# Performance work log

Hardware: AMD Instinct MI355X
Metric: run time of the kernel (lower is better)

## Reference

```python
import jax, jax.numpy as jnp
import numpy as np

DEMO_T = 4
N_HEADS = 4
N_LAYERS = 2
EPS = 1e-5
IN_DIM = 512
FF_DIM = 128
TEMP = float(np.sqrt(IN_DIM))  # temperature=None -> sqrt(in_dim)


def setup_inputs() -> dict:
    key = jax.random.key(0)
    ks = jax.random.split(key, 12)
    B, d, T, H, W = 8, IN_DIM, 36, 7, 12
    s_in = 1.0 / np.sqrt(d)
    s_ff = 1.0 / np.sqrt(FF_DIM)
    f32 = jnp.float32
    return {
        "inputs": jax.random.normal(ks[0], (B, d, T, H, W), f32),
        "demo_wq": jax.random.normal(ks[1], (N_LAYERS, FF_DIM, d), f32) * s_in,
        "demo_wk": jax.random.normal(ks[2], (N_LAYERS, FF_DIM, d), f32) * s_in,
        "demo_wv": jax.random.normal(ks[3], (N_LAYERS, FF_DIM, d), f32) * s_in,
        "demo_wo": jax.random.normal(ks[4], (N_LAYERS, d, FF_DIM), f32) * s_ff,
        "obs_wq": jax.random.normal(ks[5], (N_LAYERS, FF_DIM, d), f32) * s_in,
        "obs_wk": jax.random.normal(ks[6], (N_LAYERS, FF_DIM, d), f32) * s_in,
        "obs_wv": jax.random.normal(ks[7], (N_LAYERS, FF_DIM, d), f32) * s_in,
        "obs_wo": jax.random.normal(ks[8], (N_LAYERS, d, FF_DIM), f32) * s_ff,
        "bn_gamma": jnp.ones((N_LAYERS, d), f32),
        "bn_beta": jnp.zeros((N_LAYERS, d), f32),
    }


def _conv1x1(w, x):
    # 1x1x1 Conv3d, bias=False == per-voxel channel mixing
    return jnp.einsum('od,bdthw->bothw', w, x)


def _forward(inputs, demo_wq, demo_wk, demo_wv, demo_wo,
             obs_wq, obs_wk, obs_wv, obs_wo, bn_gamma, bn_beta):
    B, d, T, H, W = inputs.shape
    HW = H * W
    obs_T = T - DEMO_T
    neg_inf = jnp.asarray(-jnp.inf, inputs.dtype)
    # causal log-mask over demo tokens, block-expanded to spatial positions
    tril = jnp.tril(jnp.ones((DEMO_T, DEMO_T), inputs.dtype))
    mask = jnp.repeat(jnp.repeat(tril, HW, axis=0), HW, axis=1)  # (dTHW, dTHW)
    log_mask = jnp.where(mask > 0, jnp.asarray(0.0, inputs.dtype), neg_inf)

    x = inputs
    for i in range(N_LAYERS):
        demo_in = x[:, :, :DEMO_T]   # [B,d,dT,H,W]
        obs_in = x[:, :, DEMO_T:]    # [B,d,oT,H,W]

        # --- demo self-attention (causal) ---
        def demo_heads(w):
            y = _conv1x1(w, demo_in)                      # [B,ff,dT,H,W]
            return y.reshape(B, N_HEADS, -1, DEMO_T * HW)  # [B,n,ch,dTHW]
        dq, dk, dv = demo_heads(demo_wq[i]), demo_heads(demo_wk[i]), demo_heads(demo_wv[i])
        dkq = jnp.einsum('bnci,bncj->bnij', dk, dq) / TEMP + log_mask
        dattn = jax.nn.softmax(dkq, axis=-1)               # softmax over j (as in source)
        dv_att = jnp.einsum('bncj,bnij->bnci', dv, dattn)  # attended demo values
        # NOTE: the source computes demo_out via demo_Outs + relu-skip but never
        # uses it downstream (dead code); only dv_att/dk feed the obs fusion.

        # --- obs attention, fused with demo keys/attended-values ---
        def obs_heads(w):
            y = _conv1x1(w, obs_in)                        # [B,ff,oT,H,W]
            y = y.reshape(B, N_HEADS, -1, obs_T, HW)
            return jnp.transpose(y, (0, 3, 1, 2, 4))       # [B,oT,n,ch,HW]
        oq, ok, ov = obs_heads(obs_wq[i]), obs_heads(obs_wk[i]), obs_heads(obs_wv[i])
        rep_k = jnp.broadcast_to(dk[:, None], (B, obs_T) + dk.shape[1:])
        rep_v = jnp.broadcast_to(dv_att[:, None], (B, obs_T) + dv_att.shape[1:])
        cat_k = jnp.concatenate([rep_k, ok], axis=-1)      # [B,oT,n,ch,(1+dT)HW]
        cat_v = jnp.concatenate([rep_v, ov], axis=-1)
        okq = jnp.einsum('btnci,btncj->btnij', cat_k, oq) / TEMP  # i=cat len, j=HW
        oattn = jax.nn.softmax(okq, axis=-1)               # softmax over j (source: dim=4)
        ov_att = jnp.einsum('btncj,btnji->btnci', cat_v, oattn)  # [B,oT,n,ch,HW]
        obs_out = _conv1x1(obs_wo[i],
                           jnp.transpose(ov_att, (0, 2, 3, 1, 4)).reshape(B, -1, obs_T, H, W))
        # skip (out_dim == in_dim), dropout=0 -> identity
        obs_res = obs_in + jax.nn.relu(obs_out)

        # shared BatchNorm3d (training-mode batch stats) over concatenated streams
        x = jnp.concatenate([demo_in, obs_res], axis=2)
        mean = x.mean(axis=(0, 2, 3, 4)).reshape(1, -1, 1, 1, 1)
        var = x.var(axis=(0, 2, 3, 4)).reshape(1, -1, 1, 1, 1)
        g = bn_gamma[i].reshape(1, -1, 1, 1, 1)
        b = bn_beta[i].reshape(1, -1, 1, 1, 1)
        x = g * (x - mean) * jax.lax.rsqrt(var + EPS) + b
    return x  # == out_dict['last']


def reference(inputs, demo_wq, demo_wk, demo_wv, demo_wo,
              obs_wq, obs_wk, obs_wv, obs_wo, bn_gamma, bn_beta):
    return _forward(inputs, demo_wq, demo_wk, demo_wv, demo_wo,
                    obs_wq, obs_wk, obs_wv, obs_wo, bn_gamma, bn_beta)
```

## Files before the change

kernel.cpp:

```cpp
#include <hip/hip_runtime.h>

#define B_N 8
#define D_N 512
#define T_N 36
#define HW_N 84
#define THW_N 3024
#define DT_N 4
#define OT_N 32
#define NH_N 4
#define FF_N 128
#define CH_N 32
#define DI_N 336
#define OI_N 2688
#define CAT_N 420
#define INV_TEMP 0.04419417382415922f
#define BN_EPS 1e-5f
#define INV_CNT (1.0f / 24192.0f)

#define SW_DWQ 0
#define SW_DWK 131072
#define SW_DWV 262144
#define SW_OWQ 393216
#define SW_OWK 524288
#define SW_OWV 655360
#define SW_OWO 786432
#define S_DQ   917504
#define S_DK   1261568
#define S_DV   1605632
#define S_DVA  1949696
#define S_OQ   2293760
#define S_OK   5046272
#define S_OV   7798784
#define S_OVA  10551296
#define S_XBF  13303808

typedef short bf16x8 __attribute__((ext_vector_type(8)));
typedef float f32x4 __attribute__((ext_vector_type(4)));
typedef unsigned int u32;

#define GLD16(SRC, DST) __builtin_amdgcn_global_load_lds( \
    (const __attribute__((address_space(1))) u32*)(SRC), \
    (__attribute__((address_space(3))) u32*)(DST), 16, 0, 0)

__device__ __forceinline__ short f2bf(float f) {
    unsigned u = __float_as_uint(f);
    u += 0x7fffu + ((u >> 16) & 1u);
    return (short)(u >> 16);
}
__device__ __forceinline__ float bf2f(short s) {
    return __uint_as_float(((unsigned)(unsigned short)s) << 16);
}

__global__ __launch_bounds__(256) void cvt_w_kernel(
    const float* __restrict__ s0, const float* __restrict__ s1,
    const float* __restrict__ s2, const float* __restrict__ s3,
    const float* __restrict__ s4, const float* __restrict__ s5,
    const float* __restrict__ s6, short* __restrict__ dst,
    float* __restrict__ stats)
{
    const int bid = blockIdx.x;
    if (bid == 0) {
        #pragma unroll
        for (int k = 0; k < 8; ++k) stats[threadIdx.x * 8 + k] = 0.f;
    }
    const int a = bid >> 6, blk = bid & 63;
    const float* src;
    switch (a) {
        case 0: src = s0; break; case 1: src = s1; break;
        case 2: src = s2; break; case 3: src = s3; break;
        case 4: src = s4; break; case 5: src = s5; break;
        default: src = s6;
    }
    const int idx = (blk * 256 + (int)threadIdx.x) * 8;
    float4 f0 = *reinterpret_cast<const float4*>(src + idx);
    float4 f1 = *reinterpret_cast<const float4*>(src + idx + 4);
    bf16x8 pk;
    pk[0] = f2bf(f0.x); pk[1] = f2bf(f0.y); pk[2] = f2bf(f0.z); pk[3] = f2bf(f0.w);
    pk[4] = f2bf(f1.x); pk[5] = f2bf(f1.y); pk[6] = f2bf(f1.z); pk[7] = f2bf(f1.w);
    size_t dstoff;
    if (a < 6) {
        const int layer = idx >> 16;
        const int w = idx & 65535;
        const int mg = w >> 9;
        const int k  = w & 511;
        const int p  = k >> 6;
        const int kc = (k >> 3) & 7;
        const int mh = mg >> 6;
        const int m  = mg & 63;
        dstoff = (size_t)layer * 65536 +
                 (size_t)(((p * 2 + mh) * 8 + kc) * 64 + m) * 8;
    } else {
        dstoff = idx;
    }
    *reinterpret_cast<bf16x8*>(dst + (size_t)a * 131072 + dstoff) = pk;
}

__global__ __launch_bounds__(256) void xin_kernel(
    const float* __restrict__ in_f, short* __restrict__ xbf,
    float* __restrict__ stats0)
{
    __shared__ short tile[48][65];
    __shared__ float red_s[16][64];
    __shared__ float red_q[16][64];

    const int bid = blockIdx.x;
    const int b = bid / 504, rem = bid % 504, tt = rem >> 3, cblk = rem & 7;
    const int t0 = tt * 48, c0 = cblk * 64;
    const int tid = threadIdx.x;
    const bool is_demo = (tt < 7);

    #pragma unroll
    for (int l0 = 0; l0 < 768; l0 += 256) {
        int l = l0 + tid;
        int cc = l / 12, tg = l % 12;
        size_t addr = ((size_t)b * D_N + c0 + cc) * THW_N + t0 + tg * 4;
        float4 v = *reinterpret_cast<const float4*>(in_f + addr);
        tile[tg * 4 + 0][cc] = f2bf(v.x);
        tile[tg * 4 + 1][cc] = f2bf(v.y);
        tile[tg * 4 + 2][cc] = f2bf(v.z);
        tile[tg * 4 + 3][cc] = f2bf(v.w);
    }
    __syncthreads();
    float psum[4] = {}, psq[4] = {};
    const int cg = tid & 15;
    #pragma unroll
    for (int l0 = 0; l0 < 768; l0 += 256) {
        int l = l0 + tid;
        int tk = l >> 4;
        short4 s4;
        s4.x = tile[tk][cg * 4 + 0];
        s4.y = tile[tk][cg * 4 + 1];
        s4.z = tile[tk][cg * 4 + 2];
        s4.w = tile[tk][cg * 4 + 3];
        *reinterpret_cast<short4*>(
            xbf + ((size_t)b * THW_N + t0 + tk) * 512 + c0 + cg * 4) = s4;
        if (is_demo) {
            float v0 = bf2f(s4.x), v1 = bf2f(s4.y), v2 = bf2f(s4.z), v3 = bf2f(s4.w);
            psum[0] += v0; psum[1] += v1; psum[2] += v2; psum[3] += v3;
            psq[0] += v0 * v0; psq[1] += v1 * v1; psq[2] += v2 * v2; psq[3] += v3 * v3;
        }
    }
    if (!is_demo) return;
    __syncthreads();
    #pragma unroll
    for (int j = 0; j < 4; ++j) {
        red_s[tid >> 4][cg * 4 + j] = psum[j];
        red_q[tid >> 4][cg * 4 + j] = psq[j];
    }
    __syncthreads();
    if (tid < 64) {
        float s = 0.f, q = 0.f;
        #pragma unroll
        for (int r = 0; r < 16; ++r) { s += red_s[r][tid]; q += red_q[r][tid]; }
        atomicAdd(&stats0[c0 + tid], s);
        atomicAdd(&stats0[512 + c0 + tid], q);
    }
}

__global__ __launch_bounds__(256) void proj_mfma_kernel(
    const short* __restrict__ xbf, short* __restrict__ ws, int layer)
{
    __shared__ short As[3][4096];
    __shared__ short Bs[3072];

    const int tid = threadIdx.x;
    const int lane = tid & 63, wv = tid >> 6;
    const int l15 = lane & 15, q = lane >> 4;

    const int bid = blockIdx.x;
    const int mh = bid & 1;
    const int rem = bid >> 1;
    const int b = rem / 63, ct = rem - b * 63;
    const bool is_demo = (ct < 7);
    const int woff = layer * 65536;
    const short* W0 = ws + (is_demo ? SW_DWQ : SW_OWQ) + woff;
    const short* W1 = ws + (is_demo ? SW_DWK : SW_OWK) + woff;
    const short* W2 = ws + (is_demo ? SW_DWV : SW_OWV) + woff;
    const int Ltok = is_demo ? DI_N : OI_N;
    const int colL = is_demo ? ct * 48 : (ct - 7) * 48;
    short* Yq = ws + (is_demo ? S_DQ : S_OQ);
    short* Yk = ws + (is_demo ? S_DK : S_OK);
    short* Yv = ws + (is_demo ? S_DV : S_OV);
    const short* Xb = xbf + ((size_t)b * THW_N + (is_demo ? 0 : DI_N) + colL) * 512;

    const short* rp[3];
    rp[0] = W0 + (size_t)mh * 4096 + lane * 8;
    rp[1] = W1 + (size_t)mh * 4096 + lane * 8;
    rp[2] = W2 + (size_t)mh * 4096 + lane * 8;
    const short* bp[2];
    #pragma unroll
    for (int h = 0; h < 2; ++h) {
        int c = h * 192 + wv * 64 + lane;
        bp[h] = Xb + (size_t)(c % 48) * 512 + (c / 48) * 8;
    }

    f32x4 acc[3][3] = {};

    for (int k0 = 0; k0 < D_N; k0 += 64) {
        const size_t poff = (size_t)(k0 >> 6) * 8192;
        __syncthreads();
        #pragma unroll
        for (int h = 0; h < 2; ++h) {
            #pragma unroll
            for (int wt = 0; wt < 3; ++wt)
                GLD16(rp[wt] + poff + (h * 256 + wv * 64) * 8,
                      &As[wt][(h * 256 + wv * 64) * 8]);
        }
        if (wv < 3) {
            GLD16(bp[0] + k0, &Bs[(wv * 64) * 8]);
            GLD16(bp[1] + k0, &Bs[(192 + wv * 64) * 8]);
        }
        __syncthreads();

        #pragma unroll
        for (int kk = 0; kk < 2; ++kk) {
            const int kc = kk * 4 + q;
            bf16x8 bfr[3];
            #pragma unroll
            for (int nt = 0; nt < 3; ++nt)
                bfr[nt] = *reinterpret_cast<const bf16x8*>(
                    &Bs[(kc * 48 + nt * 16 + l15) * 8]);
            #pragma unroll
            for (int wt = 0; wt < 3; ++wt) {
                bf16x8 afr = *reinterpret_cast<const bf16x8*>(
                    &As[wt][(kc * 64 + wv * 16 + l15) * 8]);
                #pragma unroll
                for (int nt = 0; nt < 3; ++nt)
                    acc[wt][nt] = __builtin_amdgcn_mfma_f32_16x16x32_bf16(
                        afr, bfr[nt], acc[wt][nt], 0, 0, 0);
            }
        }
    }

    const int mrow = mh * 64 + wv * 16 + q * 4;
    #pragma unroll
    for (int nt = 0; nt < 3; ++nt) {
        const int token = colL + nt * 16 + l15;
        f32x4 aq = acc[0][nt] * INV_TEMP;
        short4 s4;
        s4.x = f2bf(aq[0]); s4.y = f2bf(aq[1]); s4.z = f2bf(aq[2]); s4.w = f2bf(aq[3]);
        *reinterpret_cast<short4*>(Yq + ((size_t)b * Ltok + token) * 128 + mrow) = s4;
        f32x4 ak = acc[1][nt];
        s4.x = f2bf(ak[0]); s4.y = f2bf(ak[1]); s4.z = f2bf(ak[2]); s4.w = f2bf(ak[3]);
        *reinterpret_cast<short4*>(Yk + ((size_t)b * Ltok + token) * 128 + mrow) = s4;
        #pragma unroll
        for (int rr = 0; rr < 4; ++rr)
            Yv[((size_t)b * FF_N + mrow + rr) * Ltok + token] = f2bf(acc[2][nt][rr]);
    }
}

template<int NT>
__device__ __forceinline__ void demo_core(
    const short* __restrict__ dqS, const short* __restrict__ dkS,
    const short* __restrict__ dvS, short* __restrict__ dvaS,
    short* __restrict__ Pt, int b, int n, int ti, int ih)
{
    constexpr int NTP = (NT + 1) & ~1;
    const int tid = threadIdx.x;
    const int lane = tid & 63, w = tid >> 6;
    const int l15 = lane & 15, q = lane >> 4;
    const int jmax = (ti + 1) * 84;

    const int irow = ih * 48 + w * 16 + l15;
    const int tokA = ti * 84 + (irow < 84 ? irow : 83);
    bf16x8 afr = *reinterpret_cast<const bf16x8*>(
        dkS + ((size_t)b * DI_N + tokA) * 128 + n * 32 + q * 8);

    f32x4 s[NT];
    #pragma unroll
    for (int nt = 0; nt < NT; ++nt) {
        bf16x8 bfr = *reinterpret_cast<const bf16x8*>(
            dqS + ((size_t)b * DI_N + nt * 16 + l15) * 128 + n * 32 + q * 8);
        f32x4 z = {};
        s[nt] = __builtin_amdgcn_mfma_f32_16x16x32_bf16(afr, bfr, z, 0, 0, 0);
    }

    const int mstart = jmax - (NT - 1) * 16;
    #pragma unroll
    for (int r = 0; r < 4; ++r) {
        if (l15 >= mstart) s[NT - 1][r] = -3.0e38f;
        float mx = s[0][r];
        #pragma unroll
        for (int nt = 1; nt < NT; ++nt) mx = fmaxf(mx, s[nt][r]);
        #pragma unroll
        for (int o = 1; o < 16; o <<= 1) mx = fmaxf(mx, __shfl_xor(mx, o));
        float sm = 0.f;
        #pragma unroll
        for (int nt = 0; nt < NT; ++nt) {
            float e = __expf(s[nt][r] - mx);
            s[nt][r] = e; sm += e;
        }
        #pragma unroll
        for (int o = 1; o < 16; o <<= 1) sm += __shfl_xor(sm, o);
        float inv = 1.f / sm;
        #pragma unroll
        for (int nt = 0; nt < NT; ++nt) s[nt][r] *= inv;
    }

    #pragma unroll
    for (int nt = 0; nt < NT; ++nt)
        #pragma unroll
        for (int r = 0; r < 4; ++r)
            Pt[(w * 16 + q * 4 + r) * 360 + nt * 16 + l15] = f2bf(s[nt][r]);
    if (NTP != NT) {
        #pragma unroll
        for (int r = 0; r < 4; ++r)
            Pt[(w * 16 + q * 4 + r) * 360 + NT * 16 + l15] = 0;
    }
    __syncthreads();

    f32x4 oacc[2] = {};
    #pragma unroll
    for (int kk = 0; kk < NTP / 2; ++kk) {
        bf16x8 pb = *reinterpret_cast<const bf16x8*>(
            &Pt[(w * 16 + l15) * 360 + kk * 32 + q * 8]);
        #pragma unroll
        for (int ct = 0; ct < 2; ++ct) {
            bf16x8 va = *reinterpret_cast<const bf16x8*>(
                dvS + ((size_t)b * FF_N + n * 32 + ct * 16 + l15) * DI_N + kk * 32 + q * 8);
            oacc[ct] = __builtin_amdgcn_mfma_f32_16x16x32_bf16(va, pb, oacc[ct], 0, 0, 0);
        }
    }

    const int ig = ih * 48 + w * 16 + l15;
    if (ig < 84) {
        #pragma unroll
        for (int ct = 0; ct < 2; ++ct)
            #pragma unroll
            for (int r = 0; r < 4; ++r)
                dvaS[((size_t)b * FF_N + n * 32 + ct * 16 + q * 4 + r) * DI_N + ti * 84 + ig] =
                    f2bf(oacc[ct][r]);
    }
}

__global__ __launch_bounds__(192) void demo_attn_mfma_kernel(const short* __restrict__ ws)
{
    __shared__ short Pt[48 * 360];

    const short* dqS = ws + S_DQ;
    const short* dkS = ws + S_DK;
    const short* dvS = ws + S_DV;
    short* dvaS = const_cast<short*>(ws) + S_DVA;

    const int bid = blockIdx.x;
    const int ih = bid & 1, ti = (bid >> 1) & 3;
    const int n = (bid >> 3) & 3, b = bid >> 5;

    switch (ti) {
        case 0: demo_core<6>(dqS, dkS, dvS, dvaS, Pt, b, n, ti, ih); break;
        case 1: demo_core<11>(dqS, dkS, dvS, dvaS, Pt, b, n, ti, ih); break;
        case 2: demo_core<16>(dqS, dkS, dvS, dvaS, Pt, b, n, ti, ih); break;
        default: demo_core<21>(dqS, dkS, dvS, dvaS, Pt, b, n, ti, ih); break;
    }
}

__global__ __launch_bounds__(256, 4) void obs_attn_mfma_kernel(const short* __restrict__ ws)
{
    __shared__ short Qt[96 * 40];
    __shared__ short Kt[64 * 40];
    __shared__ short Vs[32 * 72];
    __shared__ short Pt[96 * 72];

    const short* dkS = ws + S_DK;
    const short* dvaS = ws + S_DVA;
    const short* oqS = ws + S_OQ;
    const short* okS = ws + S_OK;
    const short* ovS = ws + S_OV;
    short* ovaS = const_cast<short*>(ws) + S_OVA;

    const int bid = blockIdx.x;
    const int b = bid >> 7, rem = bid & 127, t = rem >> 2, n = rem & 3;

    const int tid = threadIdx.x;
    const int lane = tid & 63, wv = tid >> 6;
    const int l15 = lane & 15, q = lane >> 4;

    for (int l = tid; l < 384; l += 256) {
        int i = l >> 2, c0 = (l & 3) * 8;
        bf16x8 pk = {0,0,0,0,0,0,0,0};
        if (i < HW_N)
            pk = *reinterpret_cast<const bf16x8*>(
                oqS + ((size_t)b * OI_N + t * 84 + i) * 128 + n * 32 + c0);
        *reinterpret_cast<bf16x8*>(&Qt[i * 40 + c0]) = pk;
    }

    const int pv_mt = wv & 1;
    const int pv_nb = wv >> 1;
    f32x4 oacc[3] = {};

    for (int jc = 0; jc < 448; jc += 64) {
        __syncthreads();
        {
            int jl = tid >> 2, c0 = (tid & 3) * 8;
            int jg = jc + jl;
            bf16x8 pk = {0,0,0,0,0,0,0,0};
            if (jg < DI_N)
                pk = *reinterpret_cast<const bf16x8*>(
                    dkS + ((size_t)b * DI_N + jg) * 128 + n * 32 + c0);
            else if (jg < CAT_N)
                pk = *reinterpret_cast<const bf16x8*>(
                    okS + ((size_t)b * OI_N + t * 84 + (jg - DI_N)) * 128 + n * 32 + c0);
            *reinterpret_cast<bf16x8*>(&Kt[jl * 40 + c0]) = pk;
        }
        {
            int c = tid >> 3, j0 = (tid & 7) * 8;
            int jg0 = jc + j0;
            const short* dvaRow = dvaS + ((size_t)b * FF_N + n * 32 + c) * DI_N;
            const short* ovRow = ovS + ((size_t)b * FF_N + n * 32 + c) * OI_N + t * 84;
            bf16x8 pk;
            if (jg0 + 8 <= DI_N) {
                pk = *reinterpret_cast<const bf16x8*>(dvaRow + jg0);
            } else if (jg0 >= DI_N && jg0 + 8 <= CAT_N) {
                short4 lo = *reinterpret_cast<const short4*>(ovRow + (jg0 - DI_N));
                short4 hi = *reinterpret_cast<const short4*>(ovRow + (jg0 - DI_N) + 4);
                pk[0]=lo.x; pk[1]=lo.y; pk[2]=lo.z; pk[3]=lo.w;
                pk[4]=hi.x; pk[5]=hi.y; pk[6]=hi.z; pk[7]=hi.w;
            } else {
                #pragma unroll
                for (int p = 0; p < 8; ++p) {
                    int jg = jg0 + p;
                    pk[p] = (jg < DI_N) ? dvaRow[jg]
                          : ((jg < CAT_N) ? ovRow[jg - DI_N] : (short)0);
                }
            }
            *reinterpret_cast<bf16x8*>(&Vs[c * 72 + j0]) = pk;
        }
        __syncthreads();

        f32x4 s[6];
        bf16x8 afr = *reinterpret_cast<const bf16x8*>(&Kt[(wv * 16 + l15) * 40 + q * 8]);
        #pragma unroll
        for (int nt = 0; nt < 6; ++nt) {
            bf16x8 bfr = *reinterpret_cast<const bf16x8*>(&Qt[(nt * 16 + l15) * 40 + q * 8]);
            f32x4 z = {};
            s[nt] = __builtin_amdgcn_mfma_f32_16x16x32_bf16(afr, bfr, z, 0, 0, 0);
        }
        float inv[4];
        #pragma unroll
        for (int r = 0; r < 4; ++r) {
            if (l15 >= 4) s[5][r] = -3.0e38f;
            float m2 = s[0][r];
            #pragma unroll
            for (int nt2 = 1; nt2 < 6; ++nt2) m2 = fmaxf(m2, s[nt2][r]);
            #pragma unroll
            for (int o = 1; o < 16; o <<= 1) m2 = fmaxf(m2, __shfl_xor(m2, o));
            float sm = 0.f;
            #pragma unroll
            for (int nt2 = 0; nt2 < 6; ++nt2) { float e = __expf(s[nt2][r] - m2); s[nt2][r] = e; sm += e; }
            #pragma unroll
            for (int o = 1; o < 16; o <<= 1) sm += __shfl_xor(sm, o);
            inv[r] = 1.f / sm;
        }
        #pragma unroll
        for (int nt = 0; nt < 6; ++nt) {
            short4 pk4;
            pk4.x = f2bf(s[nt][0] * inv[0]);
            pk4.y = f2bf(s[nt][1] * inv[1]);
            pk4.z = f2bf(s[nt][2] * inv[2]);
            pk4.w = f2bf(s[nt][3] * inv[3]);
            *reinterpret_cast<short4*>(&Pt[(nt * 16 + l15) * 72 + wv * 16 + q * 4]) = pk4;
        }
        __syncthreads();

        #pragma unroll
        for (int kk = 0; kk < 2; ++kk) {
            bf16x8 va = *reinterpret_cast<const bf16x8*>(&Vs[(pv_mt * 16 + l15) * 72 + kk * 32 + q * 8]);
            #pragma unroll
            for (int u = 0; u < 3; ++u) {
                int nt = pv_nb + u * 2;
                bf16x8 pb = *reinterpret_cast<const bf16x8*>(&Pt[(nt * 16 + l15) * 72 + kk * 32 + q * 8]);
                oacc[u] = __builtin_amdgcn_mfma_f32_16x16x32_bf16(va, pb, oacc[u], 0, 0, 0);
            }
        }
    }

    #pragma unroll
    for (int u = 0; u < 3; ++u) {
        int i = (pv_nb + u * 2) * 16 + l15;
        if (i < HW_N) {
            short4 st;
            st.x = f2bf(oacc[u][0]); st.y = f2bf(oacc[u][1]);
            st.z = f2bf(oacc[u][2]); st.w = f2bf(oacc[u][3]);
            *reinterpret_cast<short4*>(
                ovaS + (((size_t)b * OT_N + t) * 84 + i) * 128 + n * 32 + pv_mt * 16 + q * 4) = st;
        }
    }
}

__global__ __launch_bounds__(256) void outproj_mfma_kernel(
    short* __restrict__ xbf, const short* __restrict__ ws, int layer,
    float* __restrict__ stats)
{
    __shared__ float redS[4][32];
    __shared__ float redQ[4][32];

    const int bid = blockIdx.x;
    const int t8 = bid & 7;
    const int rr = bid >> 3;
    const int c32 = rr & 15;
    const int tc = rr >> 4;
    const int tchunk = tc * 8 + t8;
    const int o0 = c32 * 32;

    const int tid = threadIdx.x;
    const int lane = tid & 63, wv = tid >> 6;
    const int l15 = lane & 15, q = lane >> 4;

    const int g0 = tchunk * 192 + wv * 48;
    const int b = g0 / OI_N;
    const size_t xbase = (size_t)(g0 + DI_N * (b + 1)) * 512 + o0;

    const short* Wo = ws + SW_OWO + layer * 65536;
    const short* ova = ws + S_OVA;

    bf16x8 afr[2][4];
    #pragma unroll
    for (int mt = 0; mt < 2; ++mt)
        #pragma unroll
        for (int kc = 0; kc < 4; ++kc)
            afr[mt][kc] = *reinterpret_cast<const bf16x8*>(
                Wo + (size_t)(o0 + mt * 16 + l15) * FF_N + kc * 32 + q * 8);

    float csum[2][4] = {}, csq[2][4] = {};

    #pragma unroll
    for (int nt = 0; nt < 3; ++nt) {
        const int g = g0 + nt * 16;
        const short* ovaT = ova + (size_t)(g + l15) * FF_N + q * 8;
        bf16x8 bfr[4];
        #pragma unroll
        for (int kc = 0; kc < 4; ++kc)
            bfr[kc] = *reinterpret_cast<const bf16x8*>(ovaT + kc * 32);

        f32x4 acc[2] = {};
        #pragma unroll
        for (int kc = 0; kc < 4; ++kc) {
            acc[0] = __builtin_amdgcn_mfma_f32_16x16x32_bf16(afr[0][kc], bfr[kc], acc[0], 0, 0, 0);
            acc[1] = __builtin_amdgcn_mfma_f32_16x16x32_bf16(afr[1][kc], bfr[kc], acc[1], 0, 0, 0);
        }

        #pragma unroll
        for (int mt = 0; mt < 2; ++mt) {
            short* p = xbf + xbase + (size_t)(nt * 16 + l15) * 512 + mt * 16 + q * 4;
            short4 old4 = *reinterpret_cast<short4*>(p);
            float ov[4] = {bf2f(old4.x), bf2f(old4.y), bf2f(old4.z), bf2f(old4.w)};
            short4 nw;
            short* nwp = &nw.x;
            #pragma unroll
            for (int r = 0; r < 4; ++r) {
                float v = acc[mt][r];
                float y = ov[r] + (v > 0.f ? v : 0.f);
                short ybf = f2bf(y);
                nwp[r] = ybf;
                float yr = bf2f(ybf);
                csum[mt][r] += yr;
                csq[mt][r] += yr * yr;
            }
            *reinterpret_cast<short4*>(p) = nw;
        }
    }

    #pragma unroll
    for (int mt = 0; mt < 2; ++mt) {
        #pragma unroll
        for (int r = 0; r < 4; ++r) {
            float s = csum[mt][r], qq = csq[mt][r];
            #pragma unroll
            for (int o = 1; o < 16; o <<= 1) {
                s += __shfl_xor(s, o);
                qq += __shfl_xor(qq, o);
            }
            if (l15 == 0) {
                redS[wv][mt * 16 + q * 4 + r] = s;
                redQ[wv][mt * 16 + q * 4 + r] = qq;
            }
        }
    }
    __syncthreads();
    if (tid < 32) {
        float s = redS[0][tid] + redS[1][tid] + redS[2][tid] + redS[3][tid];
        float qq = redQ[0][tid] + redQ[1][tid] + redQ[2][tid] + redQ[3][tid];
        atomicAdd(&stats[o0 + tid], s);
        atomicAdd(&stats[512 + o0 + tid], qq);
    }
}

__global__ __launch_bounds__(256) void bn_mid_kernel(
    short* __restrict__ xbf, const float* __restrict__ stats,
    const float* __restrict__ gamma, const float* __restrict__ beta,
    float* __restrict__ stats_next)
{
    __shared__ float red_s[4][512];
    __shared__ float red_q[4][512];

    const int bid = blockIdx.x;
    const int b = bid / 63, tt = bid % 63;
    const int t0 = tt * 48;
    const bool is_demo = (tt < 7);
    const int tid = threadIdx.x;
    const int chg = tid & 63;
    const int trow = tid >> 6;

    float mean[8], rs[8], g[8], bb[8];
    #pragma unroll
    for (int j = 0; j < 8; ++j) {
        int c = chg * 8 + j;
        float m = stats[c] * INV_CNT;
        float var = stats[512 + c] * INV_CNT - m * m;
        mean[j] = m;
        rs[j] = rsqrtf(var + BN_EPS);
        g[j] = gamma[c];
        bb[j] = beta[c];
    }

    float psum[8] = {}, psq[8] = {};
    #pragma unroll
    for (int it = 0; it < 12; ++it) {
        int tok = t0 + it * 4 + trow;
        short* p = xbf + ((size_t)b * THW_N + tok) * 512 + chg * 8;
        bf16x8 v = *reinterpret_cast<bf16x8*>(p);
        bf16x8 w;
        #pragma unroll
        for (int j = 0; j < 8; ++j) {
            float y = g[j] * (bf2f(v[j]) - mean[j]) * rs[j] + bb[j];
            short yb = f2bf(y);
            w[j] = yb;
            if (is_demo) {
                float yr = bf2f(yb);
                psum[j] += yr; psq[j] += yr * yr;
            }
        }
        *reinterpret_cast<bf16x8*>(p) = w;
    }
    if (!is_demo) return;
    #pragma unroll
    for (int j = 0; j < 8; ++j) {
        red_s[trow][chg * 8 + j] = psum[j];
        red_q[trow][chg * 8 + j] = psq[j];
    }
    __syncthreads();
    #pragma unroll
    for (int h = 0; h < 2; ++h) {
        int c = tid + h * 256;
        float s = red_s[0][c] + red_s[1][c] + red_s[2][c] + red_s[3][c];
        float qq = red_q[0][c] + red_q[1][c] + red_q[2][c] + red_q[3][c];
        atomicAdd(&stats_next[c], s);
        atomicAdd(&stats_next[512 + c], qq);
    }
}

__global__ __launch_bounds__(256) void bn_out_kernel(
    const short* __restrict__ xbf, float* __restrict__ out_f,
    const float* __restrict__ stats,
    const float* __restrict__ gamma, const float* __restrict__ beta)
{
    __shared__ float tile[48][65];

    const int bid = blockIdx.x;
    const int b = bid / 504, rem = bid % 504, tt = rem >> 3, cblk = rem & 7;
    const int t0 = tt * 48, c0 = cblk * 64;
    const int tid = threadIdx.x;
    const int cg = tid & 15;

    float mean[4], rs[4], g[4], bb[4];
    #pragma unroll
    for (int j = 0; j < 4; ++j) {
        int c = c0 + cg * 4 + j;
        float m = stats[c] * INV_CNT;
        float var = stats[512 + c] * INV_CNT - m * m;
        mean[j] = m; rs[j] = rsqrtf(var + BN_EPS);
        g[j] = gamma[c]; bb[j] = beta[c];
    }

    #pragma unroll
    for (int l0 = 0; l0 < 768; l0 += 256) {
        int l = l0 + tid;
        int tok = l >> 4;
        short4 v = *reinterpret_cast<const short4*>(
            xbf + ((size_t)b * THW_N + t0 + tok) * 512 + c0 + cg * 4);
        tile[tok][cg * 4 + 0] = g[0] * (bf2f(v.x) - mean[0]) * rs[0] + bb[0];
        tile[tok][cg * 4 + 1] = g[1] * (bf2f(v.y) - mean[1]) * rs[1] + bb[1];
        tile[tok][cg * 4 + 2] = g[2] * (bf2f(v.z) - mean[2]) * rs[2] + bb[2];
        tile[tok][cg * 4 + 3] = g[3] * (bf2f(v.w) - mean[3]) * rs[3] + bb[3];
    }
    __syncthreads();
    #pragma unroll
    for (int l0 = 0; l0 < 768; l0 += 256) {
        int l = l0 + tid;
        int cc = l / 12, tg = l % 12;
        float4 o;
        o.x = tile[tg * 4 + 0][cc];
        o.y = tile[tg * 4 + 1][cc];
        o.z = tile[tg * 4 + 2][cc];
        o.w = tile[tg * 4 + 3][cc];
        *reinterpret_cast<float4*>(
            out_f + ((size_t)b * D_N + c0 + cc) * THW_N + t0 + tg * 4) = o;
    }
}

extern "C" void kernel_launch(void* const* d_in, const int* in_sizes, int n_in,
                              void* d_out, int out_size, void* d_ws, size_t ws_size,
                              hipStream_t stream)
{
    const float* inp  = (const float*)d_in[0];
    const float* dwq  = (const float*)d_in[1];
    const float* dwk  = (const float*)d_in[2];
    const float* dwv  = (const float*)d_in[3];
    const float* owq  = (const float*)d_in[5];
    const float* owk  = (const float*)d_in[6];
    const float* owv  = (const float*)d_in[7];
    const float* owo  = (const float*)d_in[8];
    const float* gam  = (const float*)d_in[9];
    const float* bet  = (const float*)d_in[10];
    float* x  = (float*)d_out;
    float* stats = (float*)d_ws;
    short* wsS = (short*)(stats + 2048);
    short* xbf = wsS + S_XBF;

    cvt_w_kernel<<<448, 256, 0, stream>>>(dwq, dwk, dwv, owq, owk, owv, owo, wsS, stats);
    xin_kernel<<<4032, 256, 0, stream>>>(inp, xbf, stats);

    for (int layer = 0; layer < 2; ++layer) {
        float* stL = stats + layer * 1024;
        size_t coff = (size_t)layer * D_N;
        proj_mfma_kernel<<<1008, 256, 0, stream>>>(xbf, wsS, layer);
        demo_attn_mfma_kernel<<<256, 192, 0, stream>>>(wsS);
        obs_attn_mfma_kernel<<<1024, 256, 0, stream>>>(wsS);
        outproj_mfma_kernel<<<1792, 256, 0, stream>>>(xbf, wsS, layer, stL);
        if (layer == 0) {
            bn_mid_kernel<<<504, 256, 0, stream>>>(
                xbf, stL, gam + coff, bet + coff, stats + 1024);
        } else {
            bn_out_kernel<<<4032, 256, 0, stream>>>(
                xbf, x, stL, gam + coff, bet + coff);
        }
    }
    (void)in_sizes; (void)n_in; (void)out_size; (void)ws_size;
}
```

Measured before the change: 313.7 us.

## Load obs-attention Q/K/V fragments directly from global and double-buffer P

```diff
diff --git a/kernel.cpp b/kernel.cpp
--- a/kernel.cpp
+++ b/kernel.cpp
@@ -356,10 +356,7 @@
 
 __global__ __launch_bounds__(256, 4) void obs_attn_mfma_kernel(const short* __restrict__ ws)
 {
-    __shared__ short Qt[96 * 40];
-    __shared__ short Kt[64 * 40];
-    __shared__ short Vs[32 * 72];
-    __shared__ short Pt[96 * 72];
+    __shared__ short Pt[2][96 * 72];
 
     const short* dkS = ws + S_DK;
     const short* dvaS = ws + S_DVA;
@@ -375,65 +372,38 @@
     const int lane = tid & 63, wv = tid >> 6;
     const int l15 = lane & 15, q = lane >> 4;
 
-    for (int l = tid; l < 384; l += 256) {
-        int i = l >> 2, c0 = (l & 3) * 8;
-        bf16x8 pk = {0,0,0,0,0,0,0,0};
-        if (i < HW_N)
-            pk = *reinterpret_cast<const bf16x8*>(
-                oqS + ((size_t)b * OI_N + t * 84 + i) * 128 + n * 32 + c0);
-        *reinterpret_cast<bf16x8*>(&Qt[i * 40 + c0]) = pk;
+    bf16x8 bfr[6];
+    #pragma unroll
+    for (int nt = 0; nt < 6; ++nt) {
+        int j = nt * 16 + l15; if (j > 83) j = 83;
+        bfr[nt] = *reinterpret_cast<const bf16x8*>(
+            oqS + ((size_t)b * OI_N + t * 84 + j) * 128 + n * 32 + q * 8);
     }
 
     const int pv_mt = wv & 1;
     const int pv_nb = wv >> 1;
+    const int cg = n * 32 + pv_mt * 16 + l15;
+    const short* dvaRow = dvaS + ((size_t)b * FF_N + cg) * DI_N;
+    const short* ovRow  = ovS + ((size_t)b * FF_N + cg) * OI_N + t * 84;
+
     f32x4 oacc[3] = {};
 
-    for (int jc = 0; jc < 448; jc += 64) {
-        __syncthreads();
-        {
-            int jl = tid >> 2, c0 = (tid & 3) * 8;
-            int jg = jc + jl;
-            bf16x8 pk = {0,0,0,0,0,0,0,0};
-            if (jg < DI_N)
-                pk = *reinterpret_cast<const bf16x8*>(
-                    dkS + ((size_t)b * DI_N + jg) * 128 + n * 32 + c0);
-            else if (jg < CAT_N)
-                pk = *reinterpret_cast<const bf16x8*>(
-                    okS + ((size_t)b * OI_N + t * 84 + (jg - DI_N)) * 128 + n * 32 + c0);
-            *reinterpret_cast<bf16x8*>(&Kt[jl * 40 + c0]) = pk;
-        }
-        {
-            int c = tid >> 3, j0 = (tid & 7) * 8;
-            int jg0 = jc + j0;
-            const short* dvaRow = dvaS + ((size_t)b * FF_N + n * 32 + c) * DI_N;
-            const short* ovRow = ovS + ((size_t)b * FF_N + n * 32 + c) * OI_N + t * 84;
-            bf16x8 pk;
-            if (jg0 + 8 <= DI_N) {
-                pk = *reinterpret_cast<const bf16x8*>(dvaRow + jg0);
-            } else if (jg0 >= DI_N && jg0 + 8 <= CAT_N) {
-                short4 lo = *reinterpret_cast<const short4*>(ovRow + (jg0 - DI_N));
-                short4 hi = *reinterpret_cast<const short4*>(ovRow + (jg0 - DI_N) + 4);
-                pk[0]=lo.x; pk[1]=lo.y; pk[2]=lo.z; pk[3]=lo.w;
-                pk[4]=hi.x; pk[5]=hi.y; pk[6]=hi.z; pk[7]=hi.w;
-            } else {
-                #pragma unroll
-                for (int p = 0; p < 8; ++p) {
-                    int jg = jg0 + p;
-                    pk[p] = (jg < DI_N) ? dvaRow[jg]
-                          : ((jg < CAT_N) ? ovRow[jg - DI_N] : (short)0);
-                }
-            }
-            *reinterpret_cast<bf16x8*>(&Vs[c * 72 + j0]) = pk;
-        }
-        __syncthreads();
+    #pragma unroll
+    for (int it = 0; it < 7; ++it) {
+        const int jc = it * 64;
+
+        int jg = jc + wv * 16 + l15; if (jg > 419) jg = 419;
+        bf16x8 afr = (jg < DI_N)
+            ? *reinterpret_cast<const bf16x8*>(
+                  dkS + ((size_t)b * DI_N + jg) * 128 + n * 32 + q * 8)
+            : *reinterpret_cast<const bf16x8*>(
+                  okS + ((size_t)b * OI_N + t * 84 + jg - DI_N) * 128 + n * 32 + q * 8);
 
         f32x4 s[6];
-        bf16x8 afr = *reinterpret_cast<const bf16x8*>(&Kt[(wv * 16 + l15) * 40 + q * 8]);
         #pragma unroll
         for (int nt = 0; nt < 6; ++nt) {
-            bf16x8 bfr = *reinterpret_cast<const bf16x8*>(&Qt[(nt * 16 + l15) * 40 + q * 8]);
             f32x4 z = {};
-            s[nt] = __builtin_amdgcn_mfma_f32_16x16x32_bf16(afr, bfr, z, 0, 0, 0);
+            s[nt] = __builtin_amdgcn_mfma_f32_16x16x32_bf16(afr, bfr[nt], z, 0, 0, 0);
         }
         float inv[4];
         #pragma unroll
@@ -451,24 +421,30 @@
             for (int o = 1; o < 16; o <<= 1) sm += __shfl_xor(sm, o);
             inv[r] = 1.f / sm;
         }
+        short* Pw = &Pt[it & 1][0];
+        const int ibase = jc + wv * 16 + q * 4;
         #pragma unroll
         for (int nt = 0; nt < 6; ++nt) {
             short4 pk4;
-            pk4.x = f2bf(s[nt][0] * inv[0]);
-            pk4.y = f2bf(s[nt][1] * inv[1]);
-            pk4.z = f2bf(s[nt][2] * inv[2]);
-            pk4.w = f2bf(s[nt][3] * inv[3]);
-            *reinterpret_cast<short4*>(&Pt[(nt * 16 + l15) * 72 + wv * 16 + q * 4]) = pk4;
+            pk4.x = (ibase + 0 < CAT_N) ? f2bf(s[nt][0] * inv[0]) : (short)0;
+            pk4.y = (ibase + 1 < CAT_N) ? f2bf(s[nt][1] * inv[1]) : (short)0;
+            pk4.z = (ibase + 2 < CAT_N) ? f2bf(s[nt][2] * inv[2]) : (short)0;
+            pk4.w = (ibase + 3 < CAT_N) ? f2bf(s[nt][3] * inv[3]) : (short)0;
+            *reinterpret_cast<short4*>(&Pw[(nt * 16 + l15) * 72 + wv * 16 + q * 4]) = pk4;
         }
         __syncthreads();
 
         #pragma unroll
         for (int kk = 0; kk < 2; ++kk) {
-            bf16x8 va = *reinterpret_cast<const bf16x8*>(&Vs[(pv_mt * 16 + l15) * 72 + kk * 32 + q * 8]);
+            const int i0 = jc + kk * 32 + q * 8;
+            bf16x8 va = (i0 < DI_N)
+                ? *reinterpret_cast<const bf16x8*>(dvaRow + i0)
+                : *reinterpret_cast<const bf16x8*>(ovRow + (i0 - DI_N));
             #pragma unroll
             for (int u = 0; u < 3; ++u) {
                 int nt = pv_nb + u * 2;
-                bf16x8 pb = *reinterpret_cast<const bf16x8*>(&Pt[(nt * 16 + l15) * 72 + kk * 32 + q * 8]);
+                bf16x8 pb = *reinterpret_cast<const bf16x8*>(
+                    &Pw[(nt * 16 + l15) * 72 + kk * 32 + q * 8]);
                 oacc[u] = __builtin_amdgcn_mfma_f32_16x16x32_bf16(va, pb, oacc[u], 0, 0, 0);
             }
         }
```

After: 305.1 us. 2.8% less time.
